# Kernel optimization log

Hardware: AMD Instinct MI355X
Metric: run time of the kernel (lower is better)

Reference implementation:

```python
import jax, jax.numpy as jnp
import numpy as np

NUM_CONCEPTS = 4096
CONCEPT_DIM = 512


def setup_inputs() -> dict:
    key = jax.random.key(0)
    k1, k2 = jax.random.split(key)
    inp = jax.random.normal(k1, (8, 4096, CONCEPT_DIM), dtype=jnp.float32)
    bound = 1.0 / NUM_CONCEPTS
    codebook = jax.random.uniform(
        k2, (NUM_CONCEPTS, CONCEPT_DIM), dtype=jnp.float32,
        minval=-bound, maxval=bound)
    return {"inp": inp, "codebook": codebook}


def reference(inp, codebook):
    # flatten tokens: [N, D]
    flat = inp.reshape(-1, inp.shape[-1])
    # squared Euclidean distances [N, K]; argmin is identical to cdist argmin
    d2 = (
        jnp.sum(flat * flat, axis=1, keepdims=True)
        - 2.0 * jnp.einsum("nd,kd->nk", flat, codebook)
        + jnp.sum(codebook * codebook, axis=1)[None, :]
    )
    idx = jnp.argmin(d2, axis=1)  # [N]
    quantized = jnp.take(codebook, idx, axis=0).reshape(inp.shape)
    return quantized
```

## Files before the change

kernel.cpp:

```cpp
#include <hip/hip_runtime.h>
#include <math.h>

constexpr int D  = 512;
constexpr int K  = 4096;
constexpr int BM = 64;
constexpr int BN = 64;
constexpr int BD_LEG = 32;
constexpr int PAD = 4;

#define MARGIN 2.5e-3f
constexpr int RCAP = 12;
constexpr int LCAP = 3072;

typedef short short8v __attribute__((ext_vector_type(8)));
typedef float f32x4   __attribute__((ext_vector_type(4)));
typedef int   int4v   __attribute__((ext_vector_type(4)));

constexpr size_t SC_OFF   = 0;
constexpr size_t SX_OFF   = 16384;
constexpr size_t SCS_OFF  = 147456;
constexpr size_t SXS_OFF  = 163840;
constexpr size_t CBP_OFF  = 294912;
constexpr size_t WS_NEED  = CBP_OFF + (size_t)K * D;

__device__ inline unsigned ordkey(float f) {
    unsigned u = __float_as_uint(f);
    return (u & 0x80000000u) ? ~u : (u | 0x80000000u);
}
__device__ inline float fromkey(unsigned k) {
    unsigned u = (k & 0x80000000u) ? (k ^ 0x80000000u) : ~k;
    return __uint_as_float(u);
}
__device__ inline void gload16(const void* g, void* l) {
    __builtin_amdgcn_global_load_lds(
        (const __attribute__((address_space(1))) unsigned*)g,
        (__attribute__((address_space(3))) unsigned*)l, 16, 0, 0);
}

__global__ __launch_bounds__(256)
void prep_kernel(const float* __restrict__ cb, const float* __restrict__ inp,
                 float* __restrict__ sc, float* __restrict__ scs,
                 unsigned char* __restrict__ cbp,
                 float* __restrict__ sxg, float* __restrict__ sxs,
                 unsigned char* __restrict__ ap, int nb_cb) {
    const int t = threadIdx.x;
    const bool isCB = (int)blockIdx.x < nb_cb;
    const int r = t >> 2, p = t & 3;
    const int row = (isCB ? (int)blockIdx.x : ((int)blockIdx.x - nb_cb)) * 64 + r;
    const float* base = (isCB ? cb : inp) + (size_t)row * D + p * 128;

    float s = 0.0f, m = 0.0f;
#pragma unroll
    for (int g = 0; g < 16; ++g) {
        float4 v0 = *(const float4*)(base + g * 8);
        float4 v1 = *(const float4*)(base + g * 8 + 4);
        s = fmaf(v0.x, v0.x, s); s = fmaf(v0.y, v0.y, s);
        s = fmaf(v0.z, v0.z, s); s = fmaf(v0.w, v0.w, s);
        s = fmaf(v1.x, v1.x, s); s = fmaf(v1.y, v1.y, s);
        s = fmaf(v1.z, v1.z, s); s = fmaf(v1.w, v1.w, s);
        m = fmaxf(m, fmaxf(fmaxf(fabsf(v0.x), fabsf(v0.y)), fmaxf(fabsf(v0.z), fabsf(v0.w))));
        m = fmaxf(m, fmaxf(fmaxf(fabsf(v1.x), fabsf(v1.y)), fmaxf(fabsf(v1.z), fabsf(v1.w))));
    }
    s += __shfl_xor(s, 1, 64);
    s += __shfl_xor(s, 2, 64);
    m = fmaxf(m, __shfl_xor(m, 1, 64));
    m = fmaxf(m, __shfl_xor(m, 2, 64));
    const float sinv  = (m > 0.0f) ? 127.0f / m : 0.0f;
    const float scale = m * (1.0f / 127.0f);
    if (p == 0) {
        if (isCB) { sc[row] = s;  scs[row] = scale; }
        else      { sxg[row] = s; sxs[row] = scale; }
    }

    const int rstride = isCB ? 256 : 128;
    const int tile    = isCB ? (row >> 8) : (row >> 7);
    const int rit     = isCB ? (row & 255) : (row & 127);
    unsigned char* dst = isCB ? cbp : ap;
    const size_t tbase = (size_t)tile * (32 * rstride);
#pragma unroll
    for (int g = 0; g < 16; ++g) {
        float4 v0 = *(const float4*)(base + g * 8);
        float4 v1 = *(const float4*)(base + g * 8 + 4);
        float xs[8] = {v0.x, v0.y, v0.z, v0.w, v1.x, v1.y, v1.z, v1.w};
        unsigned u0 = 0, u1 = 0;
#pragma unroll
        for (int i = 0; i < 4; ++i) {
            int q = (int)rintf(xs[i] * sinv);
            q = q > 127 ? 127 : (q < -127 ? -127 : q);
            u0 |= ((unsigned)(q & 255)) << (8 * i);
        }
#pragma unroll
        for (int i = 4; i < 8; ++i) {
            int q = (int)rintf(xs[i] * sinv);
            q = q > 127 ? 127 : (q < -127 ? -127 : q);
            u1 |= ((unsigned)(q & 255)) << (8 * (i - 4));
        }
        const int db = 2 * p + (g >> 3);
        const int j  = ((16 * p + g) >> 1) & 3;
        const size_t slot = tbase + (size_t)db * (4 * rstride) + (size_t)j * rstride + rit;
        *(unsigned*)(dst + slot * 16 + (g & 1) * 8)     = u0;
        *(unsigned*)(dst + slot * 16 + (g & 1) * 8 + 4) = u1;
    }
}

__device__ float exact_dot512(const float* __restrict__ x, const float* __restrict__ c) {
    float s = 0.0f;
#pragma unroll 4
    for (int i = 0; i < 128; ++i) {
        const float4 xv = *(const float4*)(x + i * 4);
        const float4 cv = *(const float4*)(c + i * 4);
        s = fmaf(xv.x, cv.x, s); s = fmaf(xv.y, cv.y, s);
        s = fmaf(xv.z, cv.z, s); s = fmaf(xv.w, cv.w, s);
    }
    return s;
}

__global__ __launch_bounds__(512)
void score_kernel(const unsigned char* __restrict__ a_perm,
                  const unsigned char* __restrict__ b_perm,
                  const float* __restrict__ sc, const float* __restrict__ scs,
                  const float* __restrict__ sxs,
                  char* __restrict__ records) {
    __shared__ __align__(16) unsigned char lds[2 * 24576];
    __shared__ unsigned minsh[128];
    __shared__ unsigned cntsh[128];
    __shared__ unsigned short listsh[128][RCAP];

    const int t    = threadIdx.x;
    const int lane = t & 63;
    const int w    = t >> 6;
    const int wm   = w >> 2;
    const int wn   = w & 3;
    const int l15  = lane & 15;
    const int lk   = lane >> 4;
    const int bm   = blockIdx.x >> 4;
    const int bn   = blockIdx.x & 15;

    const unsigned char* gA = a_perm + (size_t)bm * 65536  + (size_t)t * 16;
    const unsigned char* gB = b_perm + (size_t)bn * 131072 + (size_t)t * 16;

    if (t < 128) { minsh[t] = 0xFFFFFFFFu; cntsh[t] = 0u; }

    int4v acc[4][4];
#pragma unroll
    for (int i = 0; i < 4; ++i)
#pragma unroll
        for (int j = 0; j < 4; ++j) acc[i][j] = int4v{0, 0, 0, 0};

    auto STAGE = [&](int db, int dbuf) {
        gload16(gA + (size_t)db * 8192,         &lds[dbuf + t * 16]);
        gload16(gB + (size_t)db * 16384,        &lds[dbuf + 8192 + t * 16]);
        gload16(gB + (size_t)db * 16384 + 8192, &lds[dbuf + 16384 + t * 16]);
    };

    STAGE(0, 0);
    __syncthreads();

    const unsigned char* lbA = &lds[lk * 2048 + l15 * 16];
    const unsigned char* lbB = &lds[8192 + lk * 4096 + l15 * 16];
    const int mbase = wm * 1024;
    const int nbase = wn * 1024;

    auto COMPUTE = [&](int cur) {
        int4v af[4], bf[4];
#pragma unroll
        for (int mt = 0; mt < 4; ++mt)
            af[mt] = *(const int4v*)(lbA + cur + mbase + mt * 256);
#pragma unroll
        for (int nt = 0; nt < 4; ++nt)
            bf[nt] = *(const int4v*)(lbB + cur + nbase + nt * 256);
#pragma unroll
        for (int mt = 0; mt < 4; ++mt)
#pragma unroll
            for (int nt = 0; nt < 4; ++nt)
                acc[mt][nt] = __builtin_amdgcn_mfma_i32_16x16x64_i8(af[mt], bf[nt], acc[mt][nt], 0, 0, 0);
    };

    int sdb = 1;
#pragma unroll 1
    for (int p = 0; p < 4; ++p) {
        STAGE(sdb, 24576); ++sdb;
        COMPUTE(0);
        __syncthreads();
        if (p < 3) { STAGE(sdb, 0); ++sdb; }
        COMPUTE(24576);
        __syncthreads();
    }

    float scvv[4], scsv[4];
#pragma unroll
    for (int nt = 0; nt < 4; ++nt) {
        const int code = bn * 256 + wn * 64 + nt * 16 + l15;
        scvv[nt] = sc[code];
        scsv[nt] = scs[code];
    }
    float sxsv[4][4];
#pragma unroll
    for (int mt = 0; mt < 4; ++mt)
#pragma unroll
        for (int rr = 0; rr < 4; ++rr)
            sxsv[mt][rr] = sxs[bm * 128 + wm * 64 + mt * 16 + lk * 4 + rr];

#pragma unroll
    for (int mt = 0; mt < 4; ++mt)
#pragma unroll
        for (int nt = 0; nt < 4; ++nt)
#pragma unroll
            for (int rr = 0; rr < 4; ++rr) {
                const float df = (float)acc[mt][nt][rr];
                const float vv = fmaf(-2.0f * sxsv[mt][rr] * scsv[nt], df, scvv[nt]);
                acc[mt][nt][rr] = __float_as_int(vv);
            }
#define VACC(mt, nt, rr) __int_as_float(acc[mt][nt][rr])

#pragma unroll
    for (int mt = 0; mt < 4; ++mt)
#pragma unroll
        for (int rr = 0; rr < 4; ++rr) {
            float m4 = fminf(fminf(VACC(mt, 0, rr), VACC(mt, 1, rr)),
                             fminf(VACC(mt, 2, rr), VACC(mt, 3, rr)));
            m4 = fminf(m4, __shfl_xor(m4, 1, 64));
            m4 = fminf(m4, __shfl_xor(m4, 2, 64));
            m4 = fminf(m4, __shfl_xor(m4, 4, 64));
            m4 = fminf(m4, __shfl_xor(m4, 8, 64));
            if (l15 == 0) {
                const int tok = wm * 64 + mt * 16 + lk * 4 + rr;
                atomicMin(&minsh[tok], ordkey(m4));
            }
        }
    __syncthreads();

#pragma unroll
    for (int mt = 0; mt < 4; ++mt)
#pragma unroll
        for (int rr = 0; rr < 4; ++rr) {
            const int tok = wm * 64 + mt * 16 + lk * 4 + rr;
            const float tmn = fromkey(minsh[tok]) + MARGIN;
#pragma unroll
            for (int nt = 0; nt < 4; ++nt) {
                if (VACC(mt, nt, rr) <= tmn) {
                    unsigned p = atomicAdd(&cntsh[tok], 1u);
                    if (p < RCAP)
                        listsh[tok][p] = (unsigned short)(bn * 256 + wn * 64 + nt * 16 + l15);
                }
            }
        }
    __syncthreads();
#undef VACC

    if (t < 128) {
        const unsigned* lw = (const unsigned*)&listsh[t][0];
        uint4 r0, r1;
        r0.x = __float_as_uint(fromkey(minsh[t]));
        r0.y = cntsh[t];
        r0.z = lw[0]; r0.w = lw[1];
        r1.x = lw[2]; r1.y = lw[3]; r1.z = lw[4]; r1.w = lw[5];
        char* rp = records + ((size_t)(bm * 128 + t) * 16 + bn) * 32;
        *(uint4*)rp = r0;
        *(uint4*)(rp + 16) = r1;
    }
}

__global__ __launch_bounds__(256)
void resolve_kernel(const float* __restrict__ inp, const float* __restrict__ cb,
                    const float* __restrict__ sc, const float* __restrict__ sxg,
                    const char* __restrict__ records, float* __restrict__ out) {
    __shared__ unsigned long long keysh[64];
    __shared__ unsigned qtot;
    __shared__ unsigned listq[LCAP];
    __shared__ int bidx[64];

    const int t  = threadIdx.x;
    const int m0 = blockIdx.x * 64;

    if (t < 64) keysh[t] = 0xFFFFFFFFFFFFFFFFull;
    if (t == 0) qtot = 0u;
    __syncthreads();

    if (t < 64) {
        const char* rbase = records + (size_t)(m0 + t) * 16 * 32;
        float mn = __builtin_huge_valf();
#pragma unroll
        for (int i = 0; i < 16; ++i)
            mn = fminf(mn, *(const float*)(rbase + (size_t)i * 32));
        const float thr = mn + MARGIN;

        unsigned my = 0;
#pragma unroll 1
        for (int i = 0; i < 16; ++i) {
            const char* rp = rbase + (size_t)i * 32;
            if (*(const float*)rp <= thr) {
                const unsigned cnt = *(const unsigned*)(rp + 4);
                my += (cnt <= RCAP) ? cnt : 256u;
            }
        }
        unsigned pos = atomicAdd(&qtot, my);
#pragma unroll 1
        for (int i = 0; i < 16; ++i) {
            const char* rp = rbase + (size_t)i * 32;
            if (*(const float*)rp <= thr) {
                const unsigned cnt = *(const unsigned*)(rp + 4);
                if (cnt <= RCAP) {
                    const unsigned short* cs = (const unsigned short*)(rp + 8);
                    for (unsigned j = 0; j < cnt; ++j) {
                        if (pos < LCAP) listq[pos] = ((unsigned)t << 12) | cs[j];
                        ++pos;
                    }
                } else {
                    for (int c2 = 0; c2 < 256; ++c2) {
                        if (pos < LCAP) listq[pos] = ((unsigned)t << 12) | (unsigned)(i * 256 + c2);
                        ++pos;
                    }
                }
            }
        }
    }
    __syncthreads();

    const unsigned total = qtot;
    if (total <= (unsigned)LCAP) {
        for (unsigned i = t; i < total; i += 256) {
            const unsigned e = listq[i];
            const int tok  = e >> 12;
            const int code = e & 4095;
            const float dot = exact_dot512(inp + (size_t)(m0 + tok) * D, cb + (size_t)code * D);
            const float tmp = sxg[m0 + tok] - 2.0f * dot;
            const float v   = tmp + sc[code];
            const unsigned long long key =
                ((unsigned long long)__float_as_uint(v) << 32) | (unsigned)code;
            atomicMin(&keysh[tok], key);
        }
    } else {
#pragma unroll 1
        for (int tok = 0; tok < 64; ++tok) {
            const float sxv = sxg[m0 + tok];
            const float* xrow = inp + (size_t)(m0 + tok) * D;
            for (int code = t; code < K; code += 256) {
                const float dot = exact_dot512(xrow, cb + (size_t)code * D);
                const float tmp = sxv - 2.0f * dot;
                const float v   = tmp + sc[code];
                const unsigned long long key =
                    ((unsigned long long)__float_as_uint(v) << 32) | (unsigned)code;
                atomicMin(&keysh[tok], key);
            }
        }
    }
    __syncthreads();

    if (t < 64) bidx[t] = (int)(keysh[t] & 0xFFFFFFFFull);
    __syncthreads();

    for (int q = t; q < 64 * (D / 4); q += 256) {
        const int r = q >> 7;
        const int c = (q & 127) * 4;
        *(float4*)(out + (size_t)(m0 + r) * D + c) = *(const float4*)(cb + (size_t)bidx[r] * D + c);
    }
}

__global__ __launch_bounds__(256)
void sc_kernel(const float* __restrict__ cb, float* __restrict__ sc) {
    const int row  = blockIdx.x * 4 + (threadIdx.x >> 6);
    const int lane = threadIdx.x & 63;
    const float* r = cb + (size_t)row * D + lane * 8;
    float4 v0 = *(const float4*)r;
    float4 v1 = *(const float4*)(r + 4);
    float s = v0.x * v0.x;
    s += v0.y * v0.y; s += v0.z * v0.z; s += v0.w * v0.w;
    s += v1.x * v1.x; s += v1.y * v1.y; s += v1.z * v1.z; s += v1.w * v1.w;
#pragma unroll
    for (int off = 1; off < 64; off <<= 1) s += __shfl_xor(s, off, 64);
    if (lane == 0) sc[row] = s;
}

__global__ __launch_bounds__(256)
void vq_kernel(const float* __restrict__ inp, const float* __restrict__ cb,
               const float* __restrict__ sc, float* __restrict__ out) {
    __shared__ __align__(16) float As[BD_LEG][BM + PAD];
    __shared__ __align__(16) float Bs[BD_LEG][BN + PAD];
    __shared__ float sxl[BM];
    __shared__ float scs_l[BN];
    __shared__ int   bidx[BM];

    const int t  = threadIdx.x;
    const int m0 = blockIdx.x * BM;
    const int tm = t >> 4;
    const int tn = t & 15;
    const float FINF = __builtin_huge_valf();

    {
        const int r = t >> 2, p = t & 3;
        const float* row = inp + (size_t)(m0 + r) * D + p * 128;
        float s = 0.0f;
#pragma unroll
        for (int i = 0; i < 32; ++i) {
            float4 v = *(const float4*)(row + i * 4);
            s = fmaf(v.x, v.x, s); s = fmaf(v.y, v.y, s);
            s = fmaf(v.z, v.z, s); s = fmaf(v.w, v.w, s);
        }
        s += __shfl_xor(s, 1, 64);
        s += __shfl_xor(s, 2, 64);
        if (p == 0) sxl[r] = s;
    }
    __syncthreads();

    float sxm[4];
#pragma unroll
    for (int i = 0; i < 4; ++i) sxm[i] = sxl[tm * 4 + i];

    float runv[4] = {FINF, FINF, FINF, FINF};
    int   runi[4] = {0, 0, 0, 0};
    const int dq = (t & 7) << 2;
    const int mr = t >> 3;

#pragma unroll 1
    for (int kb = 0; kb < K; kb += BN) {
        __syncthreads();
        if (t < BN) scs_l[t] = sc[kb + t];

        float accl[4][4];
#pragma unroll
        for (int i = 0; i < 4; ++i)
#pragma unroll
            for (int j = 0; j < 4; ++j) accl[i][j] = 0.0f;

#pragma unroll 1
        for (int db = 0; db < D; db += BD_LEG) {
            const float* ap = inp + (size_t)(m0 + mr) * D + db + dq;
            const float* bp = cb  + (size_t)(kb + mr) * D + db + dq;
            float4 av0 = *(const float4*)ap;
            float4 av1 = *(const float4*)(ap + (size_t)32 * D);
            float4 bv0 = *(const float4*)bp;
            float4 bv1 = *(const float4*)(bp + (size_t)32 * D);
            __syncthreads();
            As[dq + 0][mr] = av0.x; As[dq + 1][mr] = av0.y;
            As[dq + 2][mr] = av0.z; As[dq + 3][mr] = av0.w;
            As[dq + 0][mr + 32] = av1.x; As[dq + 1][mr + 32] = av1.y;
            As[dq + 2][mr + 32] = av1.z; As[dq + 3][mr + 32] = av1.w;
            Bs[dq + 0][mr] = bv0.x; Bs[dq + 1][mr] = bv0.y;
            Bs[dq + 2][mr] = bv0.z; Bs[dq + 3][mr] = bv0.w;
            Bs[dq + 0][mr + 32] = bv1.x; Bs[dq + 1][mr + 32] = bv1.y;
            Bs[dq + 2][mr + 32] = bv1.z; Bs[dq + 3][mr + 32] = bv1.w;
            __syncthreads();
#pragma unroll
            for (int d = 0; d < BD_LEG; ++d) {
                const float4 a = *(const float4*)(&As[d][tm * 4]);
                const float4 b = *(const float4*)(&Bs[d][tn * 4]);
                float af[4] = {a.x, a.y, a.z, a.w};
                float bf[4] = {b.x, b.y, b.z, b.w};
#pragma unroll
                for (int i = 0; i < 4; ++i)
#pragma unroll
                    for (int j = 0; j < 4; ++j)
                        accl[i][j] = fmaf(af[i], bf[j], accl[i][j]);
            }
        }
#pragma unroll
        for (int i = 0; i < 4; ++i) {
            float bv = FINF;
            int   bi = 0x7fffffff;
#pragma unroll
            for (int j = 0; j < 4; ++j) {
                const float p = accl[i][j];
                const float tmp = sxm[i] - 2.0f * p;
                const float v   = tmp + scs_l[tn * 4 + j];
                const int  idx  = kb + tn * 4 + j;
                if (v < bv) { bv = v; bi = idx; }
            }
#pragma unroll
            for (int off = 1; off < 16; off <<= 1) {
                const float ov = __shfl_xor(bv, off, 64);
                const int   oi = __shfl_xor(bi, off, 64);
                if (ov < bv || (ov == bv && oi < bi)) { bv = ov; bi = oi; }
            }
            if (bv < runv[i]) { runv[i] = bv; runi[i] = bi; }
        }
    }
    if (tn == 0) {
#pragma unroll
        for (int i = 0; i < 4; ++i) bidx[tm * 4 + i] = runi[i];
    }
    __syncthreads();
#pragma unroll 1
    for (int q = t; q < BM * (D / 4); q += 256) {
        const int r = q >> 7;
        const int c = (q & 127) * 4;
        const float4 v = *(const float4*)(cb + (size_t)bidx[r] * D + c);
        *(float4*)(out + (size_t)(m0 + r) * D + c) = v;
    }
}

extern "C" void kernel_launch(void* const* d_in, const int* in_sizes, int n_in,
                              void* d_out, int out_size, void* d_ws, size_t ws_size,
                              hipStream_t stream) {
    const float* inp = (const float*)d_in[0];
    const float* cb  = (const float*)d_in[1];
    float* out = (float*)d_out;
    float* sc  = (float*)d_ws;
    const int tokens = in_sizes[0] / D;

    const bool fast = (ws_size >= WS_NEED) && (tokens % 256 == 0) &&
                      (in_sizes[1] == K * D) &&
                      ((size_t)out_size * 4 >= (size_t)tokens * D + (size_t)tokens * 16 * 32);

    if (fast) {
        float* sxg = (float*)((char*)d_ws + SX_OFF);
        float* scsg = (float*)((char*)d_ws + SCS_OFF);
        float* sxsg = (float*)((char*)d_ws + SXS_OFF);
        unsigned char* cbp = (unsigned char*)((char*)d_ws + CBP_OFF);
        unsigned char* ap  = (unsigned char*)d_out;
        char* records = (char*)d_out + (size_t)tokens * D;

        const int nb_cb = K / 64;

        prep_kernel<<<nb_cb + tokens / 64, 256, 0, stream>>>(cb, inp, sc, scsg, cbp,
                                                             sxg, sxsg, ap, nb_cb);
        score_kernel<<<(tokens / 128) * 16, 512, 0, stream>>>(ap, cbp, sc, scsg, sxsg, records);
        resolve_kernel<<<tokens / 64, 256, 0, stream>>>(inp, cb, sc, sxg, records, out);
    } else {
        sc_kernel<<<K / 4, 256, 0, stream>>>(cb, sc);
        vq_kernel<<<tokens / BM, 256, 0, stream>>>(inp, cb, sc, out);
    }
}
```

Before: 262.6 us.

## Coalesce int8 pack stores, parallelize record scan, shrink RCAP, cap score occupancy

The int8 quantize/pack pass in the prep kernel is restructured so each wavefront handles one row at a time with lanes covering contiguous columns and writing 8-byte stores, instead of each thread striding across 16 groups. The resolve kernel now has all 256 threads read the 16 tile records per token in parallel, with a shared atomicMin for the threshold, rather than 64 threads scanning serially. RCAP drops from 12 to 8, so records carry fewer candidates and the full 256-code fallback is taken more often. Score kernel launch bounds add a minimum of 6 blocks per SM, which may force register spilling.

Result: slower. 803.7 us (+206.1%).

```diff
diff --git a/kernel.cpp b/kernel.cpp
--- a/kernel.cpp
+++ b/kernel.cpp
@@ -9,7 +9,7 @@
 constexpr int PAD = 4;
 
 #define MARGIN 2.5e-3f
-constexpr int RCAP = 12;
+constexpr int RCAP = 8;
 constexpr int LCAP = 3072;
 
 typedef short short8v __attribute__((ext_vector_type(8)));
@@ -45,10 +45,14 @@
                  unsigned char* __restrict__ ap, int nb_cb) {
     const int t = threadIdx.x;
     const bool isCB = (int)blockIdx.x < nb_cb;
+    const int blk  = isCB ? (int)blockIdx.x : ((int)blockIdx.x - nb_cb);
+    const float* src = isCB ? cb : inp;
+    unsigned char* dst = isCB ? cbp : ap;
+    const int rstride = isCB ? 256 : 128;
+
     const int r = t >> 2, p = t & 3;
-    const int row = (isCB ? (int)blockIdx.x : ((int)blockIdx.x - nb_cb)) * 64 + r;
-    const float* base = (isCB ? cb : inp) + (size_t)row * D + p * 128;
-
+    const int row = blk * 64 + r;
+    const float* base = src + (size_t)row * D + p * 128;
     float s = 0.0f, m = 0.0f;
 #pragma unroll
     for (int g = 0; g < 16; ++g) {
@@ -72,34 +76,38 @@
         else      { sxg[row] = s; sxs[row] = scale; }
     }
 
-    const int rstride = isCB ? 256 : 128;
-    const int tile    = isCB ? (row >> 8) : (row >> 7);
-    const int rit     = isCB ? (row & 255) : (row & 127);
-    unsigned char* dst = isCB ? cbp : ap;
-    const size_t tbase = (size_t)tile * (32 * rstride);
-#pragma unroll
-    for (int g = 0; g < 16; ++g) {
-        float4 v0 = *(const float4*)(base + g * 8);
-        float4 v1 = *(const float4*)(base + g * 8 + 4);
+    const int w    = t >> 6;
+    const int lane = t & 63;
+    const int db   = lane >> 3;
+    const int j    = (lane >> 1) & 3;
+    const int half = lane & 1;
+#pragma unroll 1
+    for (int rr = 0; rr < 16; ++rr) {
+        const int row2 = blk * 64 + w * 16 + rr;
+        const float sv = __shfl(sinv, rr * 4, 64);
+        const float* rp2 = src + (size_t)row2 * D + lane * 8;
+        float4 v0 = *(const float4*)rp2;
+        float4 v1 = *(const float4*)(rp2 + 4);
         float xs[8] = {v0.x, v0.y, v0.z, v0.w, v1.x, v1.y, v1.z, v1.w};
         unsigned u0 = 0, u1 = 0;
 #pragma unroll
         for (int i = 0; i < 4; ++i) {
-            int q = (int)rintf(xs[i] * sinv);
+            int q = (int)rintf(xs[i] * sv);
             q = q > 127 ? 127 : (q < -127 ? -127 : q);
             u0 |= ((unsigned)(q & 255)) << (8 * i);
         }
 #pragma unroll
         for (int i = 4; i < 8; ++i) {
-            int q = (int)rintf(xs[i] * sinv);
+            int q = (int)rintf(xs[i] * sv);
             q = q > 127 ? 127 : (q < -127 ? -127 : q);
             u1 |= ((unsigned)(q & 255)) << (8 * (i - 4));
         }
-        const int db = 2 * p + (g >> 3);
-        const int j  = ((16 * p + g) >> 1) & 3;
-        const size_t slot = tbase + (size_t)db * (4 * rstride) + (size_t)j * rstride + rit;
-        *(unsigned*)(dst + slot * 16 + (g & 1) * 8)     = u0;
-        *(unsigned*)(dst + slot * 16 + (g & 1) * 8 + 4) = u1;
+        const int tile = row2 / rstride;
+        const int rit  = row2 % rstride;
+        const size_t slot = (size_t)tile * (32 * rstride)
+                          + (size_t)db * (4 * rstride) + (size_t)j * rstride + rit;
+        uint2 uv; uv.x = u0; uv.y = u1;
+        *(uint2*)(dst + slot * 16 + half * 8) = uv;
     }
 }
 
@@ -115,7 +123,7 @@
     return s;
 }
 
-__global__ __launch_bounds__(512)
+__global__ __launch_bounds__(512, 6)
 void score_kernel(const unsigned char* __restrict__ a_perm,
                   const unsigned char* __restrict__ b_perm,
                   const float* __restrict__ sc, const float* __restrict__ scs,
@@ -249,12 +257,14 @@
 #undef VACC
 
     if (t < 128) {
-        const unsigned* lw = (const unsigned*)&listsh[t][0];
         uint4 r0, r1;
         r0.x = __float_as_uint(fromkey(minsh[t]));
         r0.y = cntsh[t];
-        r0.z = lw[0]; r0.w = lw[1];
-        r1.x = lw[2]; r1.y = lw[3]; r1.z = lw[4]; r1.w = lw[5];
+        r0.z = (unsigned)listsh[t][0] | ((unsigned)listsh[t][1] << 16);
+        r0.w = (unsigned)listsh[t][2] | ((unsigned)listsh[t][3] << 16);
+        r1.x = (unsigned)listsh[t][4] | ((unsigned)listsh[t][5] << 16);
+        r1.y = (unsigned)listsh[t][6] | ((unsigned)listsh[t][7] << 16);
+        r1.z = 0u; r1.w = 0u;
         char* rp = records + ((size_t)(bm * 128 + t) * 16 + bn) * 32;
         *(uint4*)rp = r0;
         *(uint4*)(rp + 16) = r1;
@@ -266,51 +276,56 @@
                     const float* __restrict__ sc, const float* __restrict__ sxg,
                     const char* __restrict__ records, float* __restrict__ out) {
     __shared__ unsigned long long keysh[64];
+    __shared__ unsigned thrsh[64];
     __shared__ unsigned qtot;
     __shared__ unsigned listq[LCAP];
     __shared__ int bidx[64];
 
-    const int t  = threadIdx.x;
-    const int m0 = blockIdx.x * 64;
-
-    if (t < 64) keysh[t] = 0xFFFFFFFFFFFFFFFFull;
+    const int t   = threadIdx.x;
+    const int m0  = blockIdx.x * 64;
+    const int tok = t & 63;
+    const int q   = t >> 6;
+
+    if (t < 64) { keysh[t] = 0xFFFFFFFFFFFFFFFFull; thrsh[t] = 0xFFFFFFFFu; }
     if (t == 0) qtot = 0u;
     __syncthreads();
 
-    if (t < 64) {
-        const char* rbase = records + (size_t)(m0 + t) * 16 * 32;
+    uint4 rcA[4], rcB[4];
+    {
+        const char* rbase = records + ((size_t)(m0 + tok) * 16 + q * 4) * 32;
+#pragma unroll
+        for (int i = 0; i < 4; ++i) {
+            rcA[i] = *(const uint4*)(rbase + (size_t)i * 32);
+            rcB[i] = *(const uint4*)(rbase + (size_t)i * 32 + 16);
+        }
+    }
+    {
         float mn = __builtin_huge_valf();
 #pragma unroll
-        for (int i = 0; i < 16; ++i)
-            mn = fminf(mn, *(const float*)(rbase + (size_t)i * 32));
-        const float thr = mn + MARGIN;
-
-        unsigned my = 0;
-#pragma unroll 1
-        for (int i = 0; i < 16; ++i) {
-            const char* rp = rbase + (size_t)i * 32;
-            if (*(const float*)rp <= thr) {
-                const unsigned cnt = *(const unsigned*)(rp + 4);
-                my += (cnt <= RCAP) ? cnt : 256u;
-            }
-        }
-        unsigned pos = atomicAdd(&qtot, my);
-#pragma unroll 1
-        for (int i = 0; i < 16; ++i) {
-            const char* rp = rbase + (size_t)i * 32;
-            if (*(const float*)rp <= thr) {
-                const unsigned cnt = *(const unsigned*)(rp + 4);
-                if (cnt <= RCAP) {
-                    const unsigned short* cs = (const unsigned short*)(rp + 8);
-                    for (unsigned j = 0; j < cnt; ++j) {
-                        if (pos < LCAP) listq[pos] = ((unsigned)t << 12) | cs[j];
-                        ++pos;
-                    }
-                } else {
-                    for (int c2 = 0; c2 < 256; ++c2) {
-                        if (pos < LCAP) listq[pos] = ((unsigned)t << 12) | (unsigned)(i * 256 + c2);
-                        ++pos;
-                    }
+        for (int i = 0; i < 4; ++i) mn = fminf(mn, __uint_as_float(rcA[i].x));
+        atomicMin(&thrsh[tok], ordkey(mn));
+    }
+    __syncthreads();
+
+    const float thr = fromkey(thrsh[tok]) + MARGIN;
+#pragma unroll 1
+    for (int i = 0; i < 4; ++i) {
+        if (__uint_as_float(rcA[i].x) <= thr) {
+            const unsigned cnt = rcA[i].y;
+            if (cnt <= RCAP) {
+                const unsigned csw[4] = {rcA[i].z, rcA[i].w, rcB[i].x, rcB[i].y};
+                unsigned pos = atomicAdd(&qtot, cnt);
+                for (unsigned jj = 0; jj < cnt; ++jj) {
+                    const unsigned code = (csw[jj >> 1] >> (16 * (jj & 1))) & 0xFFFFu;
+                    if (pos < LCAP) listq[pos] = ((unsigned)tok << 12) | code;
+                    ++pos;
+                }
+            } else {
+                const int tile = q * 4 + i;
+                unsigned pos = atomicAdd(&qtot, 256u);
+                for (int c2 = 0; c2 < 256; ++c2) {
+                    if (pos < LCAP) listq[pos] = ((unsigned)tok << 12) | (unsigned)(tile * 256 + c2);
+                    ++pos;
                 }
             }
         }
@@ -321,27 +336,27 @@
     if (total <= (unsigned)LCAP) {
         for (unsigned i = t; i < total; i += 256) {
             const unsigned e = listq[i];
-            const int tok  = e >> 12;
+            const int tk   = e >> 12;
             const int code = e & 4095;
-            const float dot = exact_dot512(inp + (size_t)(m0 + tok) * D, cb + (size_t)code * D);
-            const float tmp = sxg[m0 + tok] - 2.0f * dot;
+            const float dot = exact_dot512(inp + (size_t)(m0 + tk) * D, cb + (size_t)code * D);
+            const float tmp = sxg[m0 + tk] - 2.0f * dot;
             const float v   = tmp + sc[code];
             const unsigned long long key =
                 ((unsigned long long)__float_as_uint(v) << 32) | (unsigned)code;
-            atomicMin(&keysh[tok], key);
+            atomicMin(&keysh[tk], key);
         }
     } else {
 #pragma unroll 1
-        for (int tok = 0; tok < 64; ++tok) {
-            const float sxv = sxg[m0 + tok];
-            const float* xrow = inp + (size_t)(m0 + tok) * D;
+        for (int tk = 0; tk < 64; ++tk) {
+            const float sxv = sxg[m0 + tk];
+            const float* xrow = inp + (size_t)(m0 + tk) * D;
             for (int code = t; code < K; code += 256) {
                 const float dot = exact_dot512(xrow, cb + (size_t)code * D);
                 const float tmp = sxv - 2.0f * dot;
                 const float v   = tmp + sc[code];
                 const unsigned long long key =
                     ((unsigned long long)__float_as_uint(v) << 32) | (unsigned)code;
-                atomicMin(&keysh[tok], key);
+                atomicMin(&keysh[tk], key);
             }
         }
     }
@@ -350,9 +365,9 @@
     if (t < 64) bidx[t] = (int)(keysh[t] & 0xFFFFFFFFull);
     __syncthreads();
 
-    for (int q = t; q < 64 * (D / 4); q += 256) {
-        const int r = q >> 7;
-        const int c = (q & 127) * 4;
+    for (int qq = t; qq < 64 * (D / 4); qq += 256) {
+        const int r = qq >> 7;
+        const int c = (qq & 127) * 4;
         *(float4*)(out + (size_t)(m0 + r) * D + c) = *(const float4*)(cb + (size_t)bidx[r] * D + c);
     }
 }
```
